# Kernel optimization log

Hardware: AMD Instinct MI355X
Metric: run time of the kernel (lower is better)

Reference implementation:

```python
import jax, jax.numpy as jnp
import numpy as np

B, T, C = 4, 2048, 1024
H = 16
D = C // H  # 64


def setup_inputs() -> dict:
    key = jax.random.key(0)
    k1, k2, k3 = jax.random.split(key, 3)
    x = jax.random.normal(k1, (B, T, C), dtype=jnp.float32)
    W_attn = jax.random.normal(k2, (C, 3 * C), dtype=jnp.float32) * (1.0 / np.sqrt(C))
    W_proj = jax.random.normal(k3, (C, C), dtype=jnp.float32) * (1.0 / np.sqrt(C))
    return {"x": x, "W_attn": W_attn, "W_proj": W_proj}


def reference(x, W_attn, W_proj):
    b, t, c = x.shape
    # qkv projection: [B,T,3C]
    qkv = jnp.einsum('btc,cd->btd', x, W_attn)
    q, k, v = jnp.split(qkv, 3, axis=-1)
    # split heads -> [B,H,T,D]
    q = q.reshape(b, t, H, D).transpose(0, 2, 1, 3)
    k = k.reshape(b, t, H, D).transpose(0, 2, 1, 3)
    v = v.reshape(b, t, H, D).transpose(0, 2, 1, 3)
    # scores scaled by 1/sqrt(C) (faithful to source: uses full embed dim)
    att = jnp.einsum('bhtd,bhsd->bhts', q, k) * (1.0 / jnp.sqrt(jnp.float32(c)))
    # causal mask: -inf where key index > query index
    causal = jnp.tril(jnp.ones((t, t), dtype=bool))
    att = jnp.where(causal, att, jnp.float32(-jnp.inf))
    att = jax.nn.softmax(att, axis=-1)
    # attention output -> combine heads
    y = jnp.einsum('bhts,bhsd->bhtd', att, v)
    y = y.transpose(0, 2, 1, 3).reshape(b, t, c)
    z = jnp.einsum('btc,cd->btd', y, W_proj)
    return z
```

## Files before the change

### kernel.cpp

```cpp
#include <hip/hip_runtime.h>
#include <hip/hip_bf16.h>

typedef __bf16 bf16x8 __attribute__((ext_vector_type(8)));
typedef float f32x4 __attribute__((ext_vector_type(4)));

static __device__ __forceinline__ __bf16 tobf(float x) {
    __hip_bfloat16 h = __float2bfloat16(x);
    __bf16 r;
    __builtin_memcpy(&r, &h, 2);
    return r;
}

static __device__ __forceinline__ float fexp2(float x) {
    float r;
    asm("v_exp_f32 %0, %1" : "=v"(r) : "v"(x));
    return r;
}

__global__ __launch_bounds__(256) void prep_k(const float* __restrict__ x,
                                              __hip_bfloat16* __restrict__ x_bf,
                                              const float* __restrict__ Wa,
                                              __hip_bfloat16* __restrict__ WaT,
                                              const float* __restrict__ Wp,
                                              __hip_bfloat16* __restrict__ WpT) {
    __shared__ float tile[32][33];
    const int bid = blockIdx.x;
    const int tid = threadIdx.x;
    if (bid < 8192) {
        int i = bid * 256 + tid;
        float4 v = reinterpret_cast<const float4*>(x)[i];
        __hip_bfloat16 a = __float2bfloat16(v.x);
        __hip_bfloat16 b = __float2bfloat16(v.y);
        __hip_bfloat16 c = __float2bfloat16(v.z);
        __hip_bfloat16 d = __float2bfloat16(v.w);
        ushort4 o;
        o.x = *reinterpret_cast<unsigned short*>(&a);
        o.y = *reinterpret_cast<unsigned short*>(&b);
        o.z = *reinterpret_cast<unsigned short*>(&c);
        o.w = *reinterpret_cast<unsigned short*>(&d);
        reinterpret_cast<ushort4*>(x_bf)[i] = o;
        return;
    }
    const float* in;
    __hip_bfloat16* out;
    int bx, Cn, qrows;
    float qscale;
    int t;
    if (bid < 8192 + 3072) {
        t = bid - 8192;
        in = Wa; out = WaT; Cn = 3072; qrows = 1024;
        qscale = 0.045084223f;
        bx = t % 96;
    } else {
        t = bid - 11264;
        in = Wp; out = WpT; Cn = 1024; qrows = 0;
        qscale = 1.0f;
        bx = t % 32;
    }
    const int by = (bid < 11264) ? (t / 96) : (t / 32);
    const int R = 1024;
    const int c0 = bx * 32, r0 = by * 32;
    const int tx = tid & 31, ty = tid >> 5;
#pragma unroll
    for (int i = 0; i < 4; ++i)
        tile[ty + i * 8][tx] = in[(size_t)(r0 + ty + i * 8) * Cn + c0 + tx];
    __syncthreads();
#pragma unroll
    for (int i = 0; i < 4; ++i) {
        int orow = c0 + ty + i * 8;
        float v = tile[tx][ty + i * 8];
        if (orow < qrows) v *= qscale;
        out[(size_t)orow * R + r0 + tx] = __float2bfloat16(v);
    }
}

__global__ __launch_bounds__(256) void vtrans_k(const __hip_bfloat16* __restrict__ qkv,
                                                __hip_bfloat16* __restrict__ Vt) {
    __shared__ __hip_bfloat16 tile[32][33];
    const int bh = blockIdx.z, b = bh >> 4, h = bh & 15;
    const int tt = blockIdx.x;
    const int dt = blockIdx.y;
    const int tx = threadIdx.x & 31, ty = threadIdx.x >> 5;
    const __hip_bfloat16* src = qkv + (size_t)b * 2048 * 3072 + 2048 + h * 64;
#pragma unroll
    for (int i = 0; i < 4; ++i)
        tile[ty + i * 8][tx] = src[(size_t)(tt * 32 + ty + i * 8) * 3072 + dt * 32 + tx];
    __syncthreads();
    const int slot = ((tx & 12) << 1) | (tx & 3) | ((tx >> 4) << 2);
    __hip_bfloat16* dst = Vt + ((size_t)bh * 64 + dt * 32) * 2048 + tt * 32;
#pragma unroll
    for (int i = 0; i < 4; ++i)
        dst[(size_t)(ty + i * 8) * 2048 + slot] = tile[tx][ty + i * 8];
}

template <bool OUT_BF16>
__global__ __launch_bounds__(256) void gemm_bt(const __hip_bfloat16* __restrict__ A,
                                               const __hip_bfloat16* __restrict__ Bt,
                                               __hip_bfloat16* __restrict__ Cb,
                                               float* __restrict__ Cf,
                                               int M, int N, int K) {
    __shared__ __attribute__((aligned(16))) char As[128 * 128];
    __shared__ __attribute__((aligned(16))) char Bs[128 * 128];
    const int tid = threadIdx.x;
    const int lane = tid & 63, wid = tid >> 6;
    const int l15 = lane & 15, lg = lane >> 4;
    const int wr = wid >> 1, wc = wid & 1;
    const int lin = blockIdx.y * gridDim.x + blockIdx.x;
    const int cpx = (gridDim.x * gridDim.y) >> 3;
    const int sw = (lin & 7) * cpx + (lin >> 3);
    const int bn = sw % gridDim.x, bm = sw / gridDim.x;
    const size_t arow0 = (size_t)bm * 128;
    const size_t brow0 = (size_t)bn * 128;

    f32x4 acc[4][4] = {};

    const int nk = K >> 6;
    for (int kt = 0; kt < nk; ++kt) {
        __syncthreads();
        {
            const int k0 = kt * 64;
#pragma unroll
            for (int p = 0; p < 4; ++p) {
                int idx = p * 256 + tid;
                int row = idx >> 3;
                int c = idx & 7;
                int col = 8 * (c ^ (row & 7));
                const __hip_bfloat16* ga = A + (arow0 + row) * (size_t)K + k0 + col;
                const __hip_bfloat16* gb = Bt + (brow0 + row) * (size_t)K + k0 + col;
                __builtin_amdgcn_global_load_lds(
                    (const __attribute__((address_space(1))) void*)ga,
                    (__attribute__((address_space(3))) void*)(&As[idx * 16]), 16, 0, 0);
                __builtin_amdgcn_global_load_lds(
                    (const __attribute__((address_space(1))) void*)gb,
                    (__attribute__((address_space(3))) void*)(&Bs[idx * 16]), 16, 0, 0);
            }
        }
        __syncthreads();
        const int swz = l15 & 7;
#pragma unroll
        for (int ks = 0; ks < 2; ++ks) {
            bf16x8 af[4], bfr[4];
#pragma unroll
            for (int m = 0; m < 4; ++m)
                af[m] = *reinterpret_cast<const bf16x8*>(
                    &As[(wr * 64 + m * 16 + l15) * 128 + 16 * ((ks * 4 + lg) ^ swz)]);
#pragma unroll
            for (int n = 0; n < 4; ++n)
                bfr[n] = *reinterpret_cast<const bf16x8*>(
                    &Bs[(wc * 64 + n * 16 + l15) * 128 + 16 * ((ks * 4 + lg) ^ swz)]);
#pragma unroll
            for (int m = 0; m < 4; ++m)
#pragma unroll
                for (int n = 0; n < 4; ++n)
                    acc[m][n] = __builtin_amdgcn_mfma_f32_16x16x32_bf16(af[m], bfr[n], acc[m][n], 0, 0, 0);
        }
    }

#pragma unroll
    for (int m = 0; m < 4; ++m) {
#pragma unroll
        for (int n = 0; n < 4; ++n) {
#pragma unroll
            for (int j = 0; j < 4; ++j) {
                int row = bm * 128 + wr * 64 + m * 16 + lg * 4 + j;
                int col = bn * 128 + wc * 64 + n * 16 + l15;
                if (OUT_BF16)
                    Cb[(size_t)row * N + col] = __float2bfloat16(acc[m][n][j]);
                else
                    Cf[(size_t)row * N + col] = acc[m][n][j];
            }
        }
    }
}

__global__ __launch_bounds__(256) void attn_k(const __hip_bfloat16* __restrict__ qkv,
                                              const __hip_bfloat16* __restrict__ Vt,
                                              __hip_bfloat16* __restrict__ y) {
    constexpr int TT = 2048;
    constexpr int S3C = 3072;
    const int bh = blockIdx.x, b = bh >> 4, h = bh & 15;
    const int tid = threadIdx.x;
    const int wid = tid >> 6, lane = tid & 63;
    const int l15 = lane & 15, lg = lane >> 4;

    __shared__ __attribute__((aligned(16))) char Ks[2][64 * 128];
    __shared__ __attribute__((aligned(16))) char Vs[2][64 * 128];

    const __hip_bfloat16* base = qkv + (size_t)b * TT * S3C;
    const int qo = h * 64, ko = 1024 + h * 64;
    const __hip_bfloat16* vt = Vt + (size_t)bh * 64 * TT;

    bf16x8 vones;
#pragma unroll
    for (int i = 0; i < 8; ++i) vones[i] = tobf(1.0f);

    const int idx0 = tid, idx1 = 256 + tid;
    const int r0 = idx0 >> 3, c0 = 8 * ((idx0 & 7) ^ (r0 & 7));
    const int r1 = idx1 >> 3, c1 = 8 * ((idx1 & 7) ^ (r1 & 7));

#pragma unroll 1
    for (int pass = 0; pass < 2; ++pass) {
        const int st = pass == 0 ? (15 - (int)blockIdx.y) : (int)blockIdx.y;
        const int qbase = st * 128 + wid * 32;
        const int my_nt = (qbase >> 6) + 1;
        const int blk_nt = st * 2 + 2;

        bf16x8 aq[2][2];
#pragma unroll
        for (int m = 0; m < 2; ++m) {
            const __hip_bfloat16* qp = base + (size_t)(qbase + m * 16 + l15) * S3C + qo + lg * 8;
            aq[m][0] = *reinterpret_cast<const bf16x8*>(qp);
            aq[m][1] = *reinterpret_cast<const bf16x8*>(qp + 32);
        }

        f32x4 acc[2][4] = {};
        f32x4 lsum[2] = {};

        const __hip_bfloat16* kp0 = base + (size_t)r0 * S3C + ko + c0;
        const __hip_bfloat16* kp1 = base + (size_t)r1 * S3C + ko + c1;
        const __hip_bfloat16* vp0 = vt + (size_t)r0 * TT + c0;
        const __hip_bfloat16* vp1 = vt + (size_t)r1 * TT + c1;

        auto stage = [&](int buf) {
            char* Kd = buf ? &Ks[1][0] : &Ks[0][0];
            char* Vd = buf ? &Vs[1][0] : &Vs[0][0];
            __builtin_amdgcn_global_load_lds(
                (const __attribute__((address_space(1))) void*)kp0,
                (__attribute__((address_space(3))) void*)(Kd + idx0 * 16), 16, 0, 0);
            __builtin_amdgcn_global_load_lds(
                (const __attribute__((address_space(1))) void*)kp1,
                (__attribute__((address_space(3))) void*)(Kd + idx1 * 16), 16, 0, 0);
            __builtin_amdgcn_global_load_lds(
                (const __attribute__((address_space(1))) void*)vp0,
                (__attribute__((address_space(3))) void*)(Vd + idx0 * 16), 16, 0, 0);
            __builtin_amdgcn_global_load_lds(
                (const __attribute__((address_space(1))) void*)vp1,
                (__attribute__((address_space(3))) void*)(Vd + idx1 * 16), 16, 0, 0);
            kp0 += (size_t)64 * S3C;
            kp1 += (size_t)64 * S3C;
            vp0 += 64;
            vp1 += 64;
        };

        stage(0);
        asm volatile("s_waitcnt vmcnt(0)" ::: "memory");
        __syncthreads();

        int cur = 0;
        for (int kt = 0; kt < blk_nt; ++kt) {
            if (kt + 1 < blk_nt) stage(cur ^ 1);
            if (kt < my_nt) {
                const int kb = kt * 64;
                const char* Kb = cur ? &Ks[1][0] : &Ks[0][0];
                const char* Vb = cur ? &Vs[1][0] : &Vs[0][0];
                const int swl = l15 & 7;
                f32x4 s[2][4];
                __builtin_amdgcn_s_setprio(1);
#pragma unroll
                for (int cg = 0; cg < 4; ++cg) {
                    const char* krow = Kb + (cg * 16 + l15) * 128;
                    bf16x8 k0 = *reinterpret_cast<const bf16x8*>(krow + 16 * (lg ^ swl));
                    bf16x8 k1 = *reinterpret_cast<const bf16x8*>(krow + 16 * ((4 + lg) ^ swl));
#pragma unroll
                    for (int m = 0; m < 2; ++m) {
                        f32x4 z = {0.f, 0.f, 0.f, 0.f};
                        z = __builtin_amdgcn_mfma_f32_16x16x32_bf16(k0, aq[m][0], z, 0, 0, 0);
                        z = __builtin_amdgcn_mfma_f32_16x16x32_bf16(k1, aq[m][1], z, 0, 0, 0);
                        s[m][cg] = z;
                    }
                }
                __builtin_amdgcn_s_setprio(0);
                bf16x8 vb[2][4];
#pragma unroll
                for (int dg = 0; dg < 4; ++dg) {
                    const char* vrow = Vb + (dg * 16 + l15) * 128;
                    vb[0][dg] = *reinterpret_cast<const bf16x8*>(vrow + 16 * (lg ^ swl));
                    vb[1][dg] = *reinterpret_cast<const bf16x8*>(vrow + 16 * ((4 + lg) ^ swl));
                }
                float p[2][4][4];
                const bool needmask = (kb + 63 > qbase);
#pragma unroll
                for (int m = 0; m < 2; ++m)
#pragma unroll
                    for (int cg = 0; cg < 4; ++cg)
#pragma unroll
                        for (int j = 0; j < 4; ++j) {
                            float e = fexp2(s[m][cg][j]);
                            if (needmask) {
                                int key = kb + cg * 16 + lg * 4 + j;
                                int qrow = qbase + m * 16 + l15;
                                e = (key > qrow) ? 0.f : e;
                            }
                            p[m][cg][j] = e;
                        }
                bf16x8 pa[2][2];
#pragma unroll
                for (int m = 0; m < 2; ++m)
#pragma unroll
                    for (int ks = 0; ks < 2; ++ks) {
                        bf16x8 tt2;
                        tt2[0] = tobf(p[m][2 * ks][0]);
                        tt2[1] = tobf(p[m][2 * ks][1]);
                        tt2[2] = tobf(p[m][2 * ks][2]);
                        tt2[3] = tobf(p[m][2 * ks][3]);
                        tt2[4] = tobf(p[m][2 * ks + 1][0]);
                        tt2[5] = tobf(p[m][2 * ks + 1][1]);
                        tt2[6] = tobf(p[m][2 * ks + 1][2]);
                        tt2[7] = tobf(p[m][2 * ks + 1][3]);
                        pa[m][ks] = tt2;
                    }
                __builtin_amdgcn_s_setprio(1);
#pragma unroll
                for (int ks = 0; ks < 2; ++ks) {
#pragma unroll
                    for (int dg = 0; dg < 4; ++dg)
#pragma unroll
                        for (int m = 0; m < 2; ++m)
                            acc[m][dg] = __builtin_amdgcn_mfma_f32_16x16x32_bf16(
                                pa[m][ks], vb[ks][dg], acc[m][dg], 0, 0, 0);
#pragma unroll
                    for (int m = 0; m < 2; ++m)
                        lsum[m] = __builtin_amdgcn_mfma_f32_16x16x32_bf16(pa[m][ks], vones,
                                                                          lsum[m], 0, 0, 0);
                }
                __builtin_amdgcn_s_setprio(0);
            }
            asm volatile("s_waitcnt vmcnt(0)" ::: "memory");
            __syncthreads();
            cur ^= 1;
        }

#pragma unroll
        for (int m = 0; m < 2; ++m)
#pragma unroll
            for (int j = 0; j < 4; ++j) {
                float inv = 1.f / lsum[m][j];
                int t = qbase + m * 16 + lg * 4 + j;
#pragma unroll
                for (int dg = 0; dg < 4; ++dg) {
                    float o = acc[m][dg][j] * inv;
                    y[((size_t)(b * TT + t)) * 1024 + h * 64 + dg * 16 + l15] = __float2bfloat16(o);
                }
            }
    }
}

extern "C" void kernel_launch(void* const* d_in, const int* in_sizes, int n_in,
                              void* d_out, int out_size, void* d_ws, size_t ws_size,
                              hipStream_t stream) {
    const float* x = (const float*)d_in[0];
    const float* Wa = (const float*)d_in[1];
    const float* Wp = (const float*)d_in[2];
    float* out = (float*)d_out;

    __hip_bfloat16* ws = (__hip_bfloat16*)d_ws;
    __hip_bfloat16* x_bf = ws;
    __hip_bfloat16* WaT = x_bf + (size_t)8192 * 1024;
    __hip_bfloat16* WpT = WaT + (size_t)3072 * 1024;
    __hip_bfloat16* qkv = WpT + (size_t)1024 * 1024;
    __hip_bfloat16* ybf = qkv + (size_t)8192 * 3072;
    __hip_bfloat16* Vt = x_bf;

    prep_k<<<8192 + 3072 + 1024, 256, 0, stream>>>(x, x_bf, Wa, WaT, Wp, WpT);
    gemm_bt<true><<<dim3(24, 64), 256, 0, stream>>>(x_bf, WaT, qkv, nullptr, 8192, 3072, 1024);
    vtrans_k<<<dim3(64, 2, 64), 256, 0, stream>>>(qkv, Vt);
    attn_k<<<dim3(64, 8), 256, 0, stream>>>(qkv, Vt, ybf);
    gemm_bt<false><<<dim3(8, 64), 256, 0, stream>>>(ybf, WpT, nullptr, out, 8192, 1024, 1024);
}
```

Before: 171.3 us.

## Fuse V transpose into QKV GEMM epilogue and triple-buffer attention K/V

The QKV GEMM epilogue now writes the V-section tiles straight into the transposed, slot-permuted Vt layout as packed bf16 pairs. This removes the separate vtrans kernel launch and its extra read and write of V, and Vt moves to its own workspace region. The attention kernel goes from double to triple buffering of K/V tiles, prefetching two tiles ahead and waiting on vmcnt(4) instead of draining all loads. This raises LDS use to 48KB per block, which may reduce occupancy.

```diff
diff --git a/kernel.cpp b/kernel.cpp
--- a/kernel.cpp
+++ b/kernel.cpp
@@ -9,6 +9,13 @@
     __bf16 r;
     __builtin_memcpy(&r, &h, 2);
     return r;
+}
+
+static __device__ __forceinline__ unsigned short tobits(float x) {
+    __hip_bfloat16 h = __float2bfloat16(x);
+    unsigned short u;
+    __builtin_memcpy(&u, &h, 2);
+    return u;
 }
 
 static __device__ __forceinline__ float fexp2(float x) {
@@ -74,30 +81,12 @@
     }
 }
 
-__global__ __launch_bounds__(256) void vtrans_k(const __hip_bfloat16* __restrict__ qkv,
-                                                __hip_bfloat16* __restrict__ Vt) {
-    __shared__ __hip_bfloat16 tile[32][33];
-    const int bh = blockIdx.z, b = bh >> 4, h = bh & 15;
-    const int tt = blockIdx.x;
-    const int dt = blockIdx.y;
-    const int tx = threadIdx.x & 31, ty = threadIdx.x >> 5;
-    const __hip_bfloat16* src = qkv + (size_t)b * 2048 * 3072 + 2048 + h * 64;
-#pragma unroll
-    for (int i = 0; i < 4; ++i)
-        tile[ty + i * 8][tx] = src[(size_t)(tt * 32 + ty + i * 8) * 3072 + dt * 32 + tx];
-    __syncthreads();
-    const int slot = ((tx & 12) << 1) | (tx & 3) | ((tx >> 4) << 2);
-    __hip_bfloat16* dst = Vt + ((size_t)bh * 64 + dt * 32) * 2048 + tt * 32;
-#pragma unroll
-    for (int i = 0; i < 4; ++i)
-        dst[(size_t)(ty + i * 8) * 2048 + slot] = tile[tx][ty + i * 8];
-}
-
-template <bool OUT_BF16>
+template <bool OUT_BF16, bool FUSE_VT>
 __global__ __launch_bounds__(256) void gemm_bt(const __hip_bfloat16* __restrict__ A,
                                                const __hip_bfloat16* __restrict__ Bt,
                                                __hip_bfloat16* __restrict__ Cb,
                                                float* __restrict__ Cf,
+                                               __hip_bfloat16* __restrict__ VtOut,
                                                int M, int N, int K) {
     __shared__ __attribute__((aligned(16))) char As[128 * 128];
     __shared__ __attribute__((aligned(16))) char Bs[128 * 128];
@@ -156,6 +145,27 @@
         }
     }
 
+    if (FUSE_VT && bn >= 16) {
+#pragma unroll
+        for (int m = 0; m < 4; ++m) {
+            const int rowbase = bm * 128 + wr * 64 + m * 16 + lg * 4;
+            const int bq = rowbase >> 11;
+            const int t = rowbase & 2047;
+            const int tt = t >> 5, r0 = t & 31;
+            const int slotbase = ((r0 & 12) << 1) | ((r0 >> 4) << 2);
+#pragma unroll
+            for (int n = 0; n < 4; ++n) {
+                const int col = bn * 128 + wc * 64 + n * 16 + l15;
+                const size_t vrow = (size_t)bq * 1024 + (col - 2048);
+                uint2 u;
+                u.x = (unsigned)tobits(acc[m][n][0]) | ((unsigned)tobits(acc[m][n][1]) << 16);
+                u.y = (unsigned)tobits(acc[m][n][2]) | ((unsigned)tobits(acc[m][n][3]) << 16);
+                *reinterpret_cast<uint2*>(&VtOut[vrow * 2048 + tt * 32 + slotbase]) = u;
+            }
+        }
+        return;
+    }
+
 #pragma unroll
     for (int m = 0; m < 4; ++m) {
 #pragma unroll
@@ -183,8 +193,8 @@
     const int wid = tid >> 6, lane = tid & 63;
     const int l15 = lane & 15, lg = lane >> 4;
 
-    __shared__ __attribute__((aligned(16))) char Ks[2][64 * 128];
-    __shared__ __attribute__((aligned(16))) char Vs[2][64 * 128];
+    __shared__ __attribute__((aligned(16))) char Ks[3][64 * 128];
+    __shared__ __attribute__((aligned(16))) char Vs[3][64 * 128];
 
     const __hip_bfloat16* base = qkv + (size_t)b * TT * S3C;
     const int qo = h * 64, ko = 1024 + h * 64;
@@ -222,8 +232,8 @@
         const __hip_bfloat16* vp1 = vt + (size_t)r1 * TT + c1;
 
         auto stage = [&](int buf) {
-            char* Kd = buf ? &Ks[1][0] : &Ks[0][0];
-            char* Vd = buf ? &Vs[1][0] : &Vs[0][0];
+            char* Kd = &Ks[buf][0];
+            char* Vd = &Vs[buf][0];
             __builtin_amdgcn_global_load_lds(
                 (const __attribute__((address_space(1))) void*)kp0,
                 (__attribute__((address_space(3))) void*)(Kd + idx0 * 16), 16, 0, 0);
@@ -243,16 +253,22 @@
         };
 
         stage(0);
-        asm volatile("s_waitcnt vmcnt(0)" ::: "memory");
+        stage(1);
+        asm volatile("s_waitcnt vmcnt(4)" ::: "memory");
         __syncthreads();
 
-        int cur = 0;
+        int bc = 0;
         for (int kt = 0; kt < blk_nt; ++kt) {
-            if (kt + 1 < blk_nt) stage(cur ^ 1);
+            const bool more = (kt + 2 < blk_nt);
+            if (more) {
+                int bs = bc + 2;
+                if (bs >= 3) bs -= 3;
+                stage(bs);
+            }
             if (kt < my_nt) {
                 const int kb = kt * 64;
-                const char* Kb = cur ? &Ks[1][0] : &Ks[0][0];
-                const char* Vb = cur ? &Vs[1][0] : &Vs[0][0];
+                const char* Kb = &Ks[bc][0];
+                const char* Vb = &Vs[bc][0];
                 const int swl = l15 & 7;
                 f32x4 s[2][4];
                 __builtin_amdgcn_s_setprio(1);
@@ -325,9 +341,12 @@
                 }
                 __builtin_amdgcn_s_setprio(0);
             }
-            asm volatile("s_waitcnt vmcnt(0)" ::: "memory");
+            if (more)
+                asm volatile("s_waitcnt vmcnt(4)" ::: "memory");
+            else
+                asm volatile("s_waitcnt vmcnt(0)" ::: "memory");
             __syncthreads();
-            cur ^= 1;
+            bc = (bc == 2) ? 0 : bc + 1;
         }
 
 #pragma unroll
@@ -342,6 +361,7 @@
                     y[((size_t)(b * TT + t)) * 1024 + h * 64 + dg * 16 + l15] = __float2bfloat16(o);
                 }
             }
+        __syncthreads();
     }
 }
 
@@ -359,11 +379,12 @@
     __hip_bfloat16* WpT = WaT + (size_t)3072 * 1024;
     __hip_bfloat16* qkv = WpT + (size_t)1024 * 1024;
     __hip_bfloat16* ybf = qkv + (size_t)8192 * 3072;
-    __hip_bfloat16* Vt = x_bf;
+    __hip_bfloat16* Vt = ybf + (size_t)8192 * 1024;
 
     prep_k<<<8192 + 3072 + 1024, 256, 0, stream>>>(x, x_bf, Wa, WaT, Wp, WpT);
-    gemm_bt<true><<<dim3(24, 64), 256, 0, stream>>>(x_bf, WaT, qkv, nullptr, 8192, 3072, 1024);
-    vtrans_k<<<dim3(64, 2, 64), 256, 0, stream>>>(qkv, Vt);
+    gemm_bt<true, true><<<dim3(24, 64), 256, 0, stream>>>(x_bf, WaT, qkv, nullptr, Vt,
+                                                          8192, 3072, 1024);
     attn_k<<<dim3(64, 8), 256, 0, stream>>>(qkv, Vt, ybf);
-    gemm_bt<false><<<dim3(8, 64), 256, 0, stream>>>(ybf, WpT, nullptr, out, 8192, 1024, 1024);
-}
+    gemm_bt<false, false><<<dim3(8, 64), 256, 0, stream>>>(ybf, WpT, nullptr, out, nullptr,
+                                                           8192, 1024, 1024);
+}
```

Measured after the change: 170.3 us. No clear change (-0.6%).
